# Kernel optimization log

Hardware: AMD Instinct MI355X
Metric: run time of the kernel (lower is better)

## Reference

```python
import jax, jax.numpy as jnp
import numpy as np
from jax import lax

EPS = 1e-4  # BatchNorm2d eps
K, STRIDE, PAD = 3, 1, 1


def _conv_nchw(x, w, stride, pad):
    return lax.conv_general_dilated(
        x, w, window_strides=(stride, stride), padding=[(pad, pad), (pad, pad)],
        dimension_numbers=("NCHW", "OIHW", "NCHW"))


def setup_inputs() -> dict:
    key = jax.random.key(0)
    ks = jax.random.split(key, 6)
    N, C, H, W = 16, 256, 56, 56
    Cout = 256
    return {
        "x": jax.random.normal(ks[0], (N, C, H, W), jnp.float32),
        "bn_gamma": jax.random.uniform(ks[1], (C,), jnp.float32, 0.5, 1.5),
        "bn_beta": jax.random.normal(ks[2], (C,), jnp.float32) * 0.1,
        "conv_w": jax.random.normal(ks[3], (Cout, C, K, K), jnp.float32) * (1.0 / np.sqrt(C * K * K)),
        "conv_b": jax.random.normal(ks[4], (Cout,), jnp.float32) * 0.01,
        "beta_conv_b": jax.random.normal(ks[5], (1,), jnp.float32) * 0.01,
    }


def reference(x, bn_gamma, bn_beta, conv_w, conv_b, beta_conv_b):
    # --- BatchNorm2d (training-mode batch stats, affine) ---
    mean = jnp.mean(x, axis=(0, 2, 3), keepdims=True)
    var = jnp.mean(jnp.square(x - mean), axis=(0, 2, 3), keepdims=True)  # biased
    xn = (x - mean) * lax.rsqrt(var + EPS)
    xn = xn * bn_gamma[None, :, None, None] + bn_beta[None, :, None, None]

    # --- Ternary quantize (threshold=0; le overwrites ge, so x==0 -> -1) ---
    t = jnp.where(xn >= 0.0, 1.0, 0.0)
    t = jnp.where(xn <= 0.0, -1.0, t).astype(xn.dtype)
    # scale=True, clamp=True
    xc = jnp.clip(xn, -1.0, 1.0)
    c_sum = jnp.sum(xc * t, axis=1, keepdims=True)       # [N,1,H,W]
    c_cnt = jnp.sum(jnp.abs(t), axis=1, keepdims=True)   # L1 norm over channels

    # --- Main conv on ternary activations ---
    y = _conv_nchw(t, conv_w, STRIDE, PAD) + conv_b[None, :, None, None]

    # --- beta: ones-weight box filter (+ beta_conv bias) ---
    ones_k = jnp.ones((1, 1, K, K), x.dtype)
    b_sum = _conv_nchw(c_sum, ones_k, STRIDE, PAD) + beta_conv_b[0]
    b_cnt = _conv_nchw(c_cnt, ones_k, STRIDE, PAD) + beta_conv_b[0]
    beta_map = b_sum / b_cnt                             # [N,1,Ho,Wo]
    return y * beta_map
```

## Files before the change

### kernel.cpp

```cpp
#include <hip/hip_runtime.h>
#include <hip/hip_bf16.h>

typedef __attribute__((ext_vector_type(8))) short bf16x8;
typedef __attribute__((ext_vector_type(4))) float f32x4;

#define NB 16
#define C 256
#define HH 56
#define WW 56
#define HW 3136
#define CHW 802816
#define NPIX 50176
#define PH 58
#define PW 58
#define KTOT 2304
#define PPI 3364
#define NPIXP 53824

#define GLL(g, l) __builtin_amdgcn_global_load_lds( \
    (const __attribute__((address_space(1))) void*)(g), \
    (__attribute__((address_space(3))) void*)(l), 16, 0, 0)

__global__ __launch_bounds__(1024) void stats_kernel(const float* __restrict__ x,
                             const float* __restrict__ gamma, double* __restrict__ stats) {
  int c = blockIdx.x, tid = threadIdx.x;
  double s = 0.0, s2 = 0.0;
  const float* xc = x + (size_t)c * HW;
  for (int k = tid; k < NB * (HW / 4); k += 1024) {
    int n = k / (HW / 4), i = k - n * (HW / 4);
    float4 v = *(const float4*)(xc + (size_t)n * CHW + i * 4);
    double a = v.x, b = v.y, cc = v.z, d = v.w;
    s  += (a + b) + (cc + d);
    s2 += (a * a + b * b) + (cc * cc + d * d);
  }
  __shared__ double rs[1024], rq[1024];
  rs[tid] = s; rq[tid] = s2; __syncthreads();
  for (int o = 512; o > 0; o >>= 1) {
    if (tid < o) { rs[tid] += rs[tid + o]; rq[tid] += rq[tid + o]; }
    __syncthreads();
  }
  if (tid == 0) {
    double mean = rs[0] / (double)NPIX;
    double var = rq[0] / (double)NPIX - mean * mean;
    stats[c] = mean;
    stats[C + c] = (double)gamma[c] / sqrt(var + 1e-4);
  }
}

__global__ __launch_bounds__(256) void ternarize_kernel(const float* __restrict__ x,
                                 const float* __restrict__ beta,
                                 const double* __restrict__ stats,
                                 unsigned short* __restrict__ Tp, float* __restrict__ csum) {
  int bid = blockIdx.x, tid = threadIdx.x;
  int n = bid / HH, h = bid - n * HH;
  __shared__ float xs[256][57];
  const float* xb = x + (size_t)n * CHW + h * WW;
#pragma unroll
  for (int j = 0; j < 14; ++j) {
    int idx = j * 256 + tid;
    int c = idx / 14, q = idx - c * 14;
    float4 v = *(const float4*)(xb + (size_t)c * HW + q * 4);
    float* row = &xs[c][q * 4];
    row[0] = v.x; row[1] = v.y; row[2] = v.z; row[3] = v.w;
  }
  int c8 = tid & 31;
  double mu[8], sc[8], bt[8];
#pragma unroll
  for (int e = 0; e < 8; ++e) {
    int c = c8 + 32 * e;
    mu[e] = stats[c]; sc[e] = stats[C + c]; bt[e] = (double)beta[c];
  }
  __syncthreads();
  unsigned short* tb = Tp + ((size_t)(n * PH + h + 1) * PW + 1) * C;
  float* cs = csum + (size_t)(n * PH + h + 1) * PW + 1;
#pragma unroll
  for (int p = 0; p < 7; ++p) {
    int idx = p * 256 + tid;
    int w = idx >> 5;
    unsigned bits[4];
    float msum = 0.f;
#pragma unroll
    for (int e2 = 0; e2 < 4; ++e2) {
      unsigned lo, hi;
      {
        double xn = ((double)xs[c8 + 64 * e2][w] - mu[2 * e2]) * sc[2 * e2] + bt[2 * e2];
        lo = (xn > 0.0) ? 0x3F80u : 0xBF80u;
        msum += (float)fmin(fabs(xn), 1.0);
      }
      {
        double xn = ((double)xs[c8 + 64 * e2 + 32][w] - mu[2 * e2 + 1]) * sc[2 * e2 + 1] + bt[2 * e2 + 1];
        hi = (xn > 0.0) ? 0x3F80u : 0xBF80u;
        msum += (float)fmin(fabs(xn), 1.0);
      }
      bits[e2] = lo | (hi << 16);
    }
    msum += __shfl_xor(msum, 1); msum += __shfl_xor(msum, 2);
    msum += __shfl_xor(msum, 4); msum += __shfl_xor(msum, 8);
    msum += __shfl_xor(msum, 16);
    uint4 v4; v4.x = bits[0]; v4.y = bits[1]; v4.z = bits[2]; v4.w = bits[3];
    *(uint4*)(tb + (size_t)w * C + c8 * 8) = v4;
    if (c8 == 0) cs[w] = msum;
  }
}

__global__ void prep_kernel(const float* __restrict__ cw, unsigned short* __restrict__ Wp,
                            unsigned short* __restrict__ Tp, float* __restrict__ csum) {
  int b = blockIdx.x, tid = threadIdx.x;
  if (b < 256) {
    int co = b;
    const float* src = cw + (size_t)co * KTOT;
    unsigned short* dst = Wp + (size_t)co * KTOT;
    float v[9];
#pragma unroll
    for (int t9 = 0; t9 < 9; ++t9) v[t9] = src[tid * 9 + t9];
    int p = (tid & 31) * 8 + (tid >> 5);
#pragma unroll
    for (int t9 = 0; t9 < 9; ++t9) {
      unsigned u = __builtin_bit_cast(unsigned, v[t9]);
      unsigned lsb = (u >> 16) & 1u;
      u += 0x7FFFu + lsb;
      dst[t9 * 256 + p] = (unsigned short)(u >> 16);
    }
  } else if (b < 712) {
    int g = (b - 256) * 256 + tid;
    int n = g / 7296; int r = g - n * 7296;
    int pix = r >> 5, c8 = r & 31;
    int h, w;
    if (pix < 58)      { h = 0;  w = pix; }
    else if (pix < 116){ h = 57; w = pix - 58; }
    else { int rem = pix - 116; h = 1 + (rem >> 1); w = (rem & 1) ? 57 : 0; }
    uint4 z = {0u, 0u, 0u, 0u};
    *(uint4*)(Tp + (size_t)((n * PH + h) * PW + w) * C + c8 * 8) = z;
  } else {
    int i = (b - 712) * 256 + tid;
    if (i < NPIXP) csum[i] = 0.f;
  }
}

__global__ void betamap_kernel(const float* __restrict__ csum, const float* __restrict__ betab,
                               float* __restrict__ bmap) {
  int idx = blockIdx.x * 256 + threadIdx.x;
  if (idx >= NPIX) return;
  int n = idx / HW, r = idx - n * HW;
  int h = r / WW, w = r - h * WW;
  const float* p = csum + (size_t)(n * PH + h) * PW + w;
  float s = 0.f;
  for (int i = 0; i < 3; ++i)
    for (int j = 0; j < 3; ++j) s += p[i * PW + j];
  int rows = 3 - (h == 0) - (h == HH - 1);
  int cols = 3 - (w == 0) - (w == WW - 1);
  float bb = betab[0];
  bmap[idx] = (s + bb) / (256.0f * (float)(rows * cols) + bb);
}

__global__ __launch_bounds__(256) void conv_kernel(const unsigned short* __restrict__ Wp,
    const unsigned short* __restrict__ Tp, const float* __restrict__ convb,
    const float* __restrict__ bmap, float* __restrict__ out) {
  int bid = blockIdx.x;
  int ptg = bid >> 5, xcd = bid & 7, ct = (bid >> 3) & 3;
  int pt = ptg * 8 + xcd;
  if (pt >= 211) return;
  int tid = threadIdx.x;
  int co0 = ct * 64;

  __shared__ __align__(16) unsigned short As[9 * 64 * 32];
  __shared__ __align__(16) unsigned short Bs[384 * 32];

  int aofs[9];
#pragma unroll
  for (int r = 0; r < 9; ++r) {
    int lin = r * 256 + tid;
    int co = (lin >> 2) & 63, tap = lin >> 8, pseg = lin & 3;
    int lseg = pseg ^ ((co >> 1) & 3);
    aofs[r] = (co0 + co) * KTOT + tap * 256 + lseg * 8;
  }
  int wstart = pt * 256 - 59;
  int bofs[6];
#pragma unroll
  for (int r = 0; r < 6; ++r) {
    int lin = r * 256 + tid;
    int bpix = lin >> 2, pseg = lin & 3;
    int lseg = pseg ^ ((bpix >> 1) & 3);
    int q = wstart + bpix;
    q = q < 0 ? 0 : (q >= NPIXP ? NPIXP - 1 : q);
    bofs[r] = q * C + lseg * 8;
  }

  int lane = tid & 63, wid = tid >> 6;
  int quad = lane >> 4, row16 = lane & 15;
  int aperm = (quad ^ ((row16 >> 1) & 3)) * 8;
  const unsigned short* aF = As + row16 * 32 + aperm;
  int pixb = wid * 64 + row16;

  f32x4 acc[4][4];
#pragma unroll
  for (int mi = 0; mi < 4; ++mi)
#pragma unroll
    for (int ni = 0; ni < 4; ++ni)
      acc[mi][ni] = (f32x4){0.f, 0.f, 0.f, 0.f};

  for (int c0 = 0; c0 < 256; c0 += 32) {
    __syncthreads();
#pragma unroll
    for (int r = 0; r < 9; ++r) GLL(Wp + aofs[r] + c0, As + (r * 256 + tid) * 8);
#pragma unroll
    for (int r = 0; r < 6; ++r) GLL(Tp + bofs[r] + c0, Bs + (r * 256 + tid) * 8);
    __syncthreads();
    __builtin_amdgcn_s_setprio(1);
#pragma unroll
    for (int kh = 0; kh < 3; ++kh) {
#pragma unroll
      for (int kw = 0; kw < 3; ++kw) {
        int tap = kh * 3 + kw;
        bf16x8 a[4], b[4];
#pragma unroll
        for (int mi = 0; mi < 4; ++mi)
          a[mi] = *(const bf16x8*)(aF + tap * 2048 + mi * 512);
#pragma unroll
        for (int ni = 0; ni < 4; ++ni) {
          int pix = pixb + ni * 16 + kh * 58 + kw;
          b[ni] = *(const bf16x8*)(Bs + pix * 32 + ((quad ^ ((pix >> 1) & 3)) * 8));
        }
#pragma unroll
        for (int mi = 0; mi < 4; ++mi)
#pragma unroll
          for (int ni = 0; ni < 4; ++ni)
            acc[mi][ni] = __builtin_amdgcn_mfma_f32_16x16x32_bf16(a[mi], b[ni], acc[mi][ni], 0, 0, 0);
      }
    }
    __builtin_amdgcn_s_setprio(0);
  }

#pragma unroll
  for (int ni = 0; ni < 4; ++ni) {
    int pp = pt * 256 + wid * 64 + ni * 16 + row16;
    if (pp >= NPIXP) continue;
    int n = pp / PPI; int r = pp - n * PPI;
    int ph = r / PW;  int pw = r - ph * PW;
    if (ph < 1 || ph > 56 || pw < 1 || pw > 56) continue;
    int pix = (ph - 1) * WW + (pw - 1);
    float bm = bmap[n * HW + pix];
    float* ob = out + (size_t)n * CHW + pix;
#pragma unroll
    for (int mi = 0; mi < 4; ++mi) {
      int co = co0 + mi * 16 + quad * 4;
#pragma unroll
      for (int rg = 0; rg < 4; ++rg) {
        ob[(size_t)(co + rg) * HW] = (acc[mi][ni][rg] + convb[co + rg]) * bm;
      }
    }
  }
}

extern "C" void kernel_launch(void* const* d_in, const int* in_sizes, int n_in,
                              void* d_out, int out_size, void* d_ws, size_t ws_size,
                              hipStream_t stream) {
  const float* x     = (const float*)d_in[0];
  const float* gamma = (const float*)d_in[1];
  const float* beta  = (const float*)d_in[2];
  const float* convw = (const float*)d_in[3];
  const float* convb = (const float*)d_in[4];
  const float* betab = (const float*)d_in[5];
  float* out = (float*)d_out;

  char* ws = (char*)d_ws;
  unsigned short* Tp   = (unsigned short*)(ws);
  unsigned short* Wp   = (unsigned short*)(ws + 27557888);
  float*          csum = (float*)(ws + 28737536);
  float*          bmap = (float*)(ws + 28952832);
  double*         stats= (double*)(ws + 29153536);

  prep_kernel<<<923, 256, 0, stream>>>(convw, Wp, Tp, csum);
  stats_kernel<<<256, 1024, 0, stream>>>(x, gamma, stats);
  ternarize_kernel<<<896, 256, 0, stream>>>(x, beta, stats, Tp, csum);
  betamap_kernel<<<196, 256, 0, stream>>>(csum, betab, bmap);
  conv_kernel<<<864, 256, 0, stream>>>(Wp, Tp, convb, bmap, out);
}
```

Baseline: 188.6 us.

## Double-buffer conv LDS tiles, enlarge pixel tile, fuse beta-map into epilogue

The conv kernel now runs 512-thread blocks, each covering 512 padded pixels. Its A and B LDS tiles are double-buffered so the global-to-LDS loads for the next channel chunk are issued while MFMAs run on the current one, with one barrier per step. The separate betamap kernel is removed: each output pixel's 3x3 box sum and normalisation is computed in the conv epilogue straight from csum. This saves a launch and a global round-trip. The cost is about 155 KB of LDS per block, which likely limits each CU to one block and makes the 424 active blocks fill the CUs unevenly.

```diff
diff --git a/kernel.cpp b/kernel.cpp
--- a/kernel.cpp
+++ b/kernel.cpp
@@ -137,48 +137,33 @@
   }
 }
 
-__global__ void betamap_kernel(const float* __restrict__ csum, const float* __restrict__ betab,
-                               float* __restrict__ bmap) {
-  int idx = blockIdx.x * 256 + threadIdx.x;
-  if (idx >= NPIX) return;
-  int n = idx / HW, r = idx - n * HW;
-  int h = r / WW, w = r - h * WW;
-  const float* p = csum + (size_t)(n * PH + h) * PW + w;
-  float s = 0.f;
-  for (int i = 0; i < 3; ++i)
-    for (int j = 0; j < 3; ++j) s += p[i * PW + j];
-  int rows = 3 - (h == 0) - (h == HH - 1);
-  int cols = 3 - (w == 0) - (w == WW - 1);
-  float bb = betab[0];
-  bmap[idx] = (s + bb) / (256.0f * (float)(rows * cols) + bb);
-}
-
-__global__ __launch_bounds__(256) void conv_kernel(const unsigned short* __restrict__ Wp,
+__global__ __launch_bounds__(512, 2) void conv_kernel(const unsigned short* __restrict__ Wp,
     const unsigned short* __restrict__ Tp, const float* __restrict__ convb,
-    const float* __restrict__ bmap, float* __restrict__ out) {
+    const float* __restrict__ csum, const float* __restrict__ betab,
+    float* __restrict__ out) {
   int bid = blockIdx.x;
   int ptg = bid >> 5, xcd = bid & 7, ct = (bid >> 3) & 3;
   int pt = ptg * 8 + xcd;
-  if (pt >= 211) return;
+  if (pt >= 106) return;
   int tid = threadIdx.x;
   int co0 = ct * 64;
 
-  __shared__ __align__(16) unsigned short As[9 * 64 * 32];
-  __shared__ __align__(16) unsigned short Bs[384 * 32];
-
-  int aofs[9];
-#pragma unroll
-  for (int r = 0; r < 9; ++r) {
-    int lin = r * 256 + tid;
+  __shared__ __align__(16) unsigned short As[2][18432];
+  __shared__ __align__(16) unsigned short Bs[2][20480];
+
+  int aofs[5];
+#pragma unroll
+  for (int r = 0; r < 5; ++r) {
+    int lin = r * 512 + tid;
     int co = (lin >> 2) & 63, tap = lin >> 8, pseg = lin & 3;
     int lseg = pseg ^ ((co >> 1) & 3);
     aofs[r] = (co0 + co) * KTOT + tap * 256 + lseg * 8;
   }
-  int wstart = pt * 256 - 59;
-  int bofs[6];
-#pragma unroll
-  for (int r = 0; r < 6; ++r) {
-    int lin = r * 256 + tid;
+  int wstart = pt * 512 - 59;
+  int bofs[5];
+#pragma unroll
+  for (int r = 0; r < 5; ++r) {
+    int lin = r * 512 + tid;
     int bpix = lin >> 2, pseg = lin & 3;
     int lseg = pseg ^ ((bpix >> 1) & 3);
     int q = wstart + bpix;
@@ -188,8 +173,7 @@
 
   int lane = tid & 63, wid = tid >> 6;
   int quad = lane >> 4, row16 = lane & 15;
-  int aperm = (quad ^ ((row16 >> 1) & 3)) * 8;
-  const unsigned short* aF = As + row16 * 32 + aperm;
+  int aFoff = row16 * 32 + (quad ^ ((row16 >> 1) & 3)) * 8;
   int pixb = wid * 64 + row16;
 
   f32x4 acc[4][4];
@@ -199,13 +183,25 @@
     for (int ni = 0; ni < 4; ++ni)
       acc[mi][ni] = (f32x4){0.f, 0.f, 0.f, 0.f};
 
-  for (int c0 = 0; c0 < 256; c0 += 32) {
+#pragma unroll
+  for (int r = 0; r < 4; ++r) GLL(Wp + aofs[r], &As[0][(r * 512 + tid) * 8]);
+  if (tid < 256)               GLL(Wp + aofs[4], &As[0][(2048 + tid) * 8]);
+#pragma unroll
+  for (int r = 0; r < 5; ++r) GLL(Tp + bofs[r], &Bs[0][(r * 512 + tid) * 8]);
+
+  for (int s = 0; s < 8; ++s) {
+    int cur = s & 1;
     __syncthreads();
-#pragma unroll
-    for (int r = 0; r < 9; ++r) GLL(Wp + aofs[r] + c0, As + (r * 256 + tid) * 8);
-#pragma unroll
-    for (int r = 0; r < 6; ++r) GLL(Tp + bofs[r] + c0, Bs + (r * 256 + tid) * 8);
-    __syncthreads();
+    if (s < 7) {
+      int c0n = (s + 1) * 32;
+#pragma unroll
+      for (int r = 0; r < 4; ++r) GLL(Wp + aofs[r] + c0n, &As[cur ^ 1][(r * 512 + tid) * 8]);
+      if (tid < 256)               GLL(Wp + aofs[4] + c0n, &As[cur ^ 1][(2048 + tid) * 8]);
+#pragma unroll
+      for (int r = 0; r < 5; ++r) GLL(Tp + bofs[r] + c0n, &Bs[cur ^ 1][(r * 512 + tid) * 8]);
+    }
+    const unsigned short* aB = &As[cur][0];
+    const unsigned short* bB = &Bs[cur][0];
     __builtin_amdgcn_s_setprio(1);
 #pragma unroll
     for (int kh = 0; kh < 3; ++kh) {
@@ -215,11 +211,11 @@
         bf16x8 a[4], b[4];
 #pragma unroll
         for (int mi = 0; mi < 4; ++mi)
-          a[mi] = *(const bf16x8*)(aF + tap * 2048 + mi * 512);
+          a[mi] = *(const bf16x8*)(aB + tap * 2048 + mi * 512 + aFoff);
 #pragma unroll
         for (int ni = 0; ni < 4; ++ni) {
           int pix = pixb + ni * 16 + kh * 58 + kw;
-          b[ni] = *(const bf16x8*)(Bs + pix * 32 + ((quad ^ ((pix >> 1) & 3)) * 8));
+          b[ni] = *(const bf16x8*)(bB + pix * 32 + ((quad ^ ((pix >> 1) & 3)) * 8));
         }
 #pragma unroll
         for (int mi = 0; mi < 4; ++mi)
@@ -231,15 +227,24 @@
     __builtin_amdgcn_s_setprio(0);
   }
 
+  float bb = betab[0];
 #pragma unroll
   for (int ni = 0; ni < 4; ++ni) {
-    int pp = pt * 256 + wid * 64 + ni * 16 + row16;
+    int pp = pt * 512 + wid * 64 + ni * 16 + row16;
     if (pp >= NPIXP) continue;
-    int n = pp / PPI; int r = pp - n * PPI;
-    int ph = r / PW;  int pw = r - ph * PW;
+    int n = pp / PPI; int r2 = pp - n * PPI;
+    int ph = r2 / PW;  int pw = r2 - ph * PW;
     if (ph < 1 || ph > 56 || pw < 1 || pw > 56) continue;
+    const float* cp = csum + (size_t)(n * PH + ph - 1) * PW + (pw - 1);
+    float s9 = 0.f;
+#pragma unroll
+    for (int i = 0; i < 3; ++i)
+#pragma unroll
+      for (int j = 0; j < 3; ++j) s9 += cp[i * PW + j];
+    int rows = 3 - (ph == 1) - (ph == 56);
+    int cols = 3 - (pw == 1) - (pw == 56);
+    float bm = (s9 + bb) / (256.0f * (float)(rows * cols) + bb);
     int pix = (ph - 1) * WW + (pw - 1);
-    float bm = bmap[n * HW + pix];
     float* ob = out + (size_t)n * CHW + pix;
 #pragma unroll
     for (int mi = 0; mi < 4; ++mi) {
@@ -267,12 +272,10 @@
   unsigned short* Tp   = (unsigned short*)(ws);
   unsigned short* Wp   = (unsigned short*)(ws + 27557888);
   float*          csum = (float*)(ws + 28737536);
-  float*          bmap = (float*)(ws + 28952832);
   double*         stats= (double*)(ws + 29153536);
 
   prep_kernel<<<923, 256, 0, stream>>>(convw, Wp, Tp, csum);
   stats_kernel<<<256, 1024, 0, stream>>>(x, gamma, stats);
   ternarize_kernel<<<896, 256, 0, stream>>>(x, beta, stats, Tp, csum);
-  betamap_kernel<<<196, 256, 0, stream>>>(csum, betab, bmap);
-  conv_kernel<<<864, 256, 0, stream>>>(Wp, Tp, convb, bmap, out);
-}
+  conv_kernel<<<448, 512, 0, stream>>>(Wp, Tp, convb, csum, betab, out);
+}
```

Result: slower. 195.7 us (+3.8%).
